# Optimization experiments

Hardware: AMD Instinct MI355X
Metric: run time of the kernel (lower is better)

## Reference

```python
import jax, jax.numpy as jnp
import numpy as np

B, N, D, E, H, K = 2, 2048, 1024, 8, 2048, 2


def setup_inputs() -> dict:
    key = jax.random.key(0)
    ks = jax.random.split(key, 5)
    s = 0.02  # init scale
    return {
        "x": jax.random.normal(ks[0], (B, N, D), dtype=jnp.float32),
        "w_gate": jax.random.normal(ks[1], (D, E), dtype=jnp.float32) * s,
        "b_gate": jnp.zeros((E,), dtype=jnp.float32),
        "w1": jax.random.normal(ks[2], (E, D, H), dtype=jnp.float32) * s,
        "b1": jnp.zeros((E, H), dtype=jnp.float32),
        "w2": jax.random.normal(ks[3], (E, H, D), dtype=jnp.float32) * s,
        "b2": jnp.zeros((E, D), dtype=jnp.float32),
    }


def reference(x, w_gate, b_gate, w1, b1, w2, b2):
    b, n, d = x.shape
    T = b * n
    xf = x.reshape(T, d)                                   # (T, D)
    # --- top-k routing ---
    logits = xf @ w_gate + b_gate                          # (T, E)
    topk_logits, topk_idx = jax.lax.top_k(logits, K)       # (T, K)
    topk_gates = jax.nn.softmax(topk_logits, axis=-1)      # softmax over selected experts
    entropy = -(topk_gates * jnp.log(jnp.clip(topk_gates, 1e-8, None))).sum(-1).mean()
    # scatter top-k gates into full (T, E) gate matrix (zeros for unselected)
    gates = jnp.zeros_like(logits).at[jnp.arange(T)[:, None], topk_idx].add(topk_gates)
    # --- expert MLPs (dense over experts; gates zero out unselected) ---
    h = jax.nn.relu(jnp.einsum('td,edh->eth', xf, w1) + b1[:, None, :])  # (E, T, H)
    y = jnp.einsum('eth,ehd->etd', h, w2) + b2[:, None, :]               # (E, T, D)
    out = jnp.einsum('etd,te->td', y, gates).reshape(b, n, d)
    return out, entropy
```

## Files before the change

### kernel.cpp

```cpp
#include <hip/hip_runtime.h>

#define T_TOK 4096
#define D_DIM 1024
#define E_EXP 8
#define H_DIM 2048
#define CAP   9216
#define TILES_M 72

typedef __attribute__((ext_vector_type(8))) short bf16x8;
typedef __attribute__((ext_vector_type(4))) float f32x4;

__device__ inline unsigned short f2bf(float f) {
    unsigned int u = __float_as_uint(f);
    unsigned int r = (u + 0x7fffu + ((u >> 16) & 1u)) >> 16;
    return (unsigned short)r;
}

#define GLD_LDS16(g, l)                                                        \
    __builtin_amdgcn_global_load_lds(                                          \
        (const __attribute__((address_space(1))) void*)(g),                    \
        (__attribute__((address_space(3))) void*)(l), 16, 0, 0)

__global__ __launch_bounds__(256) void tcvt_kernel(const float* __restrict__ src,
                                                   unsigned short* __restrict__ dst,
                                                   int R, int C) {
    __shared__ float tile[64][65];
    size_t eo = (size_t)blockIdx.z * R * C;
    src += eo; dst += eo;
    int tx = threadIdx.x & 15, ty = threadIdx.x >> 4;
    int c0 = blockIdx.x * 64, r0 = blockIdx.y * 64;
    #pragma unroll
    for (int i = 0; i < 4; i++) {
        int row = ty + i * 16;
        float4 v = *(const float4*)&src[(size_t)(r0 + row) * C + c0 + tx * 4];
        tile[row][tx * 4 + 0] = v.x;
        tile[row][tx * 4 + 1] = v.y;
        tile[row][tx * 4 + 2] = v.z;
        tile[row][tx * 4 + 3] = v.w;
    }
    __syncthreads();
    #pragma unroll
    for (int i = 0; i < 4; i++) {
        int cc = ty + i * 16;
        int rr = tx * 4;
        ushort4 o;
        o.x = f2bf(tile[rr + 0][cc]);
        o.y = f2bf(tile[rr + 1][cc]);
        o.z = f2bf(tile[rr + 2][cc]);
        o.w = f2bf(tile[rr + 3][cc]);
        *(ushort4*)&dst[(size_t)(c0 + cc) * R + r0 + rr] = o;
    }
}

__global__ __launch_bounds__(256) void gating_kernel(
    const float* __restrict__ xf, const float* __restrict__ wg,
    const float* __restrict__ bg, unsigned short* __restrict__ xb,
    int* __restrict__ tk_e, float* __restrict__ tk_g,
    float* __restrict__ ent_part)
{
    __shared__ float ents[4];
    int wave = threadIdx.x >> 6, lane = threadIdx.x & 63;
    int t = blockIdx.x * 4 + wave;
    const float* xr = xf + (size_t)t * D_DIM;
    unsigned short* xbr = xb + (size_t)t * D_DIM;
    float acc[8] = {0.f,0.f,0.f,0.f,0.f,0.f,0.f,0.f};
    for (int i = 0; i < 16; i++) {
        int d = lane + i * 64;
        float xv = xr[d];
        xbr[d] = f2bf(xv);
        const float4* wr = (const float4*)(wg + (size_t)d * 8);
        float4 w0 = wr[0], w1 = wr[1];
        acc[0] += xv * w0.x; acc[1] += xv * w0.y; acc[2] += xv * w0.z; acc[3] += xv * w0.w;
        acc[4] += xv * w1.x; acc[5] += xv * w1.y; acc[6] += xv * w1.z; acc[7] += xv * w1.w;
    }
    #pragma unroll
    for (int s = 1; s < 64; s <<= 1) {
        #pragma unroll
        for (int e = 0; e < 8; e++) acc[e] += __shfl_xor(acc[e], s, 64);
    }
    if (lane == 0) {
        float l[8];
        #pragma unroll
        for (int e = 0; e < 8; e++) l[e] = acc[e] + bg[e];
        int i0 = 0;
        #pragma unroll
        for (int e = 1; e < 8; e++) if (l[e] > l[i0]) i0 = e;
        int i1 = (i0 == 0) ? 1 : 0;
        #pragma unroll
        for (int e = 0; e < 8; e++) if (e != i0 && l[e] > l[i1]) i1 = e;
        float z  = expf(l[i1] - l[i0]);
        float p0 = 1.0f / (1.0f + z);
        float p1 = z / (1.0f + z);
        float ent = -(p0 * logf(fmaxf(p0, 1e-8f)) + p1 * logf(fmaxf(p1, 1e-8f)));
        ents[wave] = ent;
        tk_e[t * 2 + 0] = i0; tk_g[t * 2 + 0] = p0;
        tk_e[t * 2 + 1] = i1; tk_g[t * 2 + 1] = p1;
    }
    __syncthreads();
    if (threadIdx.x == 0)
        ent_part[blockIdx.x] = ents[0] + ents[1] + ents[2] + ents[3];
}

__global__ __launch_bounds__(1024) void route_kernel(
    const int* __restrict__ tk_e, const float* __restrict__ tk_g,
    int* __restrict__ off, int* __restrict__ slot_token,
    float* __restrict__ slot_gate, int* __restrict__ slot_of,
    const float* __restrict__ ent_part, float* __restrict__ ent_out)
{
    __shared__ int wt[16][8];
    __shared__ int wx[16][8];
    __shared__ int base[9];
    __shared__ int tot[8];
    __shared__ float es[16];

    int tid = threadIdx.x, wid = tid >> 6, lane = tid & 63;
    int i0 = tid * 8;
    int ev[8];
    *(int4*)&ev[0] = *(const int4*)&tk_e[i0];
    *(int4*)&ev[4] = *(const int4*)&tk_e[i0 + 4];

    float s = ent_part[tid];
    #pragma unroll
    for (int d = 1; d < 64; d <<= 1) s += __shfl_xor(s, d, 64);
    if (lane == 0) es[wid] = s;

    unsigned own[4] = {0u, 0u, 0u, 0u};
    #pragma unroll
    for (int j = 0; j < 8; j++) {
        int e = ev[j];
        int reg = ((e < 4) ? 0 : 2) + (e & 1);
        own[reg] += 1u << (((e >> 1) & 1) * 16);
    }
    unsigned inc[4] = {own[0], own[1], own[2], own[3]};
    #pragma unroll
    for (int d = 1; d < 64; d <<= 1) {
        #pragma unroll
        for (int k = 0; k < 4; k++) {
            unsigned t = __shfl_up(inc[k], d, 64);
            if (lane >= d) inc[k] += t;
        }
    }
    if (lane == 63) {
        #pragma unroll
        for (int e = 0; e < 8; e++) {
            int reg = ((e < 4) ? 0 : 2) + (e & 1);
            wt[wid][e] = (inc[reg] >> (((e >> 1) & 1) * 16)) & 0xFFFF;
        }
    }
    __syncthreads();
    if (tid == 0) {
        int o = 0;
        for (int e = 0; e < 8; e++) {
            int run = 0;
            for (int w = 0; w < 16; w++) { wx[w][e] = run; run += wt[w][e]; }
            tot[e] = run;
            base[e] = o;
            off[e] = o;
            o += (run + 127) & ~127;
        }
        base[8] = o;
        off[8] = o;
        float se = 0.f;
        for (int w = 0; w < 16; w++) se += es[w];
        *ent_out = se * (1.0f / T_TOK);
    }
    __syncthreads();

    #pragma unroll
    for (int e = 0; e < 8; e++) {
        int p0 = base[e] + tot[e], p1 = base[e + 1];
        for (int i = p0 + tid; i < p1; i += 1024) slot_token[i] = -1;
    }

    unsigned run[4] = {0u, 0u, 0u, 0u};
    #pragma unroll
    for (int j = 0; j < 8; j++) {
        int e = ev[j];
        int reg = ((e < 4) ? 0 : 2) + (e & 1);
        int sh = ((e >> 1) & 1) * 16;
        int lx = (int)(((inc[reg] - own[reg]) >> sh) & 0xFFFF);
        int lr = (int)((run[reg] >> sh) & 0xFFFF);
        int slot = base[e] + wx[wid][e] + lx + lr;
        run[reg] += 1u << sh;
        int i = i0 + j;
        slot_token[slot] = i >> 1;
        slot_gate[slot] = tk_g[i];
        slot_of[i] = slot;
    }
}

__global__ __launch_bounds__(256) void gemm1_kernel(
    const unsigned short* __restrict__ xb, const unsigned short* __restrict__ w1t,
    const float* __restrict__ b1g, const int* __restrict__ off,
    const int* __restrict__ slot_token, unsigned short* __restrict__ Hb)
{
    __shared__ __align__(16) unsigned short As[128 * 32];
    __shared__ __align__(16) unsigned short Bs[128 * 32];

    int s0 = blockIdx.x * 128;
    if (s0 >= off[E_EXP]) return;
    int e = 0;
    while (s0 >= off[e + 1]) e++;
    int n0 = blockIdx.y * 128;

    int tid = threadIdx.x;
    int wave = tid >> 6, lane = tid & 63;
    int lrow = lane & 15, quad = lane >> 4;
    int srow = lane >> 2;
    int scol = ((lane & 3) ^ ((srow >> 1) & 3)) * 8;

    int r0 = 16 * wave + srow, r1 = r0 + 64;
    int t0 = slot_token[s0 + r0]; if (t0 < 0) t0 = 0;
    int t1 = slot_token[s0 + r1]; if (t1 < 0) t1 = 0;
    const unsigned short* wb = w1t + (size_t)e * H_DIM * D_DIM;
    const unsigned short* a0 = xb + (size_t)t0 * D_DIM + scol;
    const unsigned short* a1 = xb + (size_t)t1 * D_DIM + scol;
    const unsigned short* bp0 = wb + (size_t)(n0 + r0) * D_DIM + scol;
    const unsigned short* bp1 = wb + (size_t)(n0 + r1) * D_DIM + scol;

    unsigned short* lA0 = As + (16 * wave) * 32;
    unsigned short* lA1 = As + (64 + 16 * wave) * 32;
    unsigned short* lB0 = Bs + (16 * wave) * 32;
    unsigned short* lB1 = Bs + (64 + 16 * wave) * 32;

    f32x4 acc[4][4];
    #pragma unroll
    for (int mi = 0; mi < 4; mi++)
        #pragma unroll
        for (int ni = 0; ni < 4; ni++) acc[mi][ni] = (f32x4){0.f, 0.f, 0.f, 0.f};

    int wr = (wave >> 1) * 64, wc = (wave & 1) * 64;
    int g = (quad ^ ((lrow >> 1) & 3)) * 8;

    for (int k0 = 0; k0 < D_DIM; k0 += 32) {
        __syncthreads();
        GLD_LDS16(a0 + k0, lA0);
        GLD_LDS16(a1 + k0, lA1);
        GLD_LDS16(bp0 + k0, lB0);
        GLD_LDS16(bp1 + k0, lB1);
        __syncthreads();
        bf16x8 af[4], bfr[4];
        #pragma unroll
        for (int i = 0; i < 4; i++) {
            af[i]  = *(const bf16x8*)&As[(wr + i * 16 + lrow) * 32 + g];
            bfr[i] = *(const bf16x8*)&Bs[(wc + i * 16 + lrow) * 32 + g];
        }
        #pragma unroll
        for (int mi = 0; mi < 4; mi++)
            #pragma unroll
            for (int ni = 0; ni < 4; ni++)
                acc[mi][ni] = __builtin_amdgcn_mfma_f32_16x16x32_bf16(
                    af[mi], bfr[ni], acc[mi][ni], 0, 0, 0);
    }

    float bv[4];
    #pragma unroll
    for (int ni = 0; ni < 4; ni++) bv[ni] = b1g[e * H_DIM + n0 + wc + ni * 16 + lrow];
    unsigned short* w = As + wave * 1024;
    __syncthreads();
    #pragma unroll
    for (int mi = 0; mi < 4; mi++) {
        #pragma unroll
        for (int ni = 0; ni < 4; ni++)
            #pragma unroll
            for (int r = 0; r < 4; r++)
                w[(quad * 4 + r) * 64 + ni * 16 + lrow] =
                    f2bf(fmaxf(acc[mi][ni][r] + bv[ni], 0.0f));
        int rd = lane >> 3, cc = (lane & 7) * 8;
        bf16x8 v0 = *(const bf16x8*)&w[rd * 64 + cc];
        bf16x8 v1 = *(const bf16x8*)&w[(8 + rd) * 64 + cc];
        size_t rowg = (size_t)(s0 + wr + mi * 16 + rd) * H_DIM + n0 + wc + cc;
        *(bf16x8*)&Hb[rowg] = v0;
        *(bf16x8*)&Hb[rowg + 8 * H_DIM] = v1;
    }
}

__global__ __launch_bounds__(256) void gemm2_kernel(
    const unsigned short* __restrict__ Hb, const unsigned short* __restrict__ w2t,
    const float* __restrict__ b2g, const int* __restrict__ off,
    unsigned short* __restrict__ Yb)
{
    __shared__ __align__(16) unsigned short As[128 * 32];
    __shared__ __align__(16) unsigned short Bs[128 * 32];

    int s0 = blockIdx.x * 128;
    if (s0 >= off[E_EXP]) return;
    int e = 0;
    while (s0 >= off[e + 1]) e++;
    int n0 = blockIdx.y * 128;

    int tid = threadIdx.x;
    int wave = tid >> 6, lane = tid & 63;
    int lrow = lane & 15, quad = lane >> 4;
    int srow = lane >> 2;
    int scol = ((lane & 3) ^ ((srow >> 1) & 3)) * 8;

    int r0 = 16 * wave + srow, r1 = r0 + 64;
    const unsigned short* wb = w2t + (size_t)e * D_DIM * H_DIM;
    const unsigned short* a0 = Hb + (size_t)(s0 + r0) * H_DIM + scol;
    const unsigned short* a1 = Hb + (size_t)(s0 + r1) * H_DIM + scol;
    const unsigned short* bp0 = wb + (size_t)(n0 + r0) * H_DIM + scol;
    const unsigned short* bp1 = wb + (size_t)(n0 + r1) * H_DIM + scol;

    unsigned short* lA0 = As + (16 * wave) * 32;
    unsigned short* lA1 = As + (64 + 16 * wave) * 32;
    unsigned short* lB0 = Bs + (16 * wave) * 32;
    unsigned short* lB1 = Bs + (64 + 16 * wave) * 32;

    f32x4 acc[4][4];
    #pragma unroll
    for (int mi = 0; mi < 4; mi++)
        #pragma unroll
        for (int ni = 0; ni < 4; ni++) acc[mi][ni] = (f32x4){0.f, 0.f, 0.f, 0.f};

    int wr = (wave >> 1) * 64, wc = (wave & 1) * 64;
    int g = (quad ^ ((lrow >> 1) & 3)) * 8;

    for (int k0 = 0; k0 < H_DIM; k0 += 32) {
        __syncthreads();
        GLD_LDS16(a0 + k0, lA0);
        GLD_LDS16(a1 + k0, lA1);
        GLD_LDS16(bp0 + k0, lB0);
        GLD_LDS16(bp1 + k0, lB1);
        __syncthreads();
        bf16x8 af[4], bfr[4];
        #pragma unroll
        for (int i = 0; i < 4; i++) {
            af[i]  = *(const bf16x8*)&As[(wr + i * 16 + lrow) * 32 + g];
            bfr[i] = *(const bf16x8*)&Bs[(wc + i * 16 + lrow) * 32 + g];
        }
        #pragma unroll
        for (int mi = 0; mi < 4; mi++)
            #pragma unroll
            for (int ni = 0; ni < 4; ni++)
                acc[mi][ni] = __builtin_amdgcn_mfma_f32_16x16x32_bf16(
                    af[mi], bfr[ni], acc[mi][ni], 0, 0, 0);
    }

    float bv[4];
    #pragma unroll
    for (int ni = 0; ni < 4; ni++) bv[ni] = b2g[e * D_DIM + n0 + wc + ni * 16 + lrow];
    unsigned short* w = As + wave * 1024;
    __syncthreads();
    #pragma unroll
    for (int mi = 0; mi < 4; mi++) {
        #pragma unroll
        for (int ni = 0; ni < 4; ni++)
            #pragma unroll
            for (int r = 0; r < 4; r++)
                w[(quad * 4 + r) * 64 + ni * 16 + lrow] = f2bf(acc[mi][ni][r] + bv[ni]);
        int rd = lane >> 3, cc = (lane & 7) * 8;
        bf16x8 v0 = *(const bf16x8*)&w[rd * 64 + cc];
        bf16x8 v1 = *(const bf16x8*)&w[(8 + rd) * 64 + cc];
        size_t rowg = (size_t)(s0 + wr + mi * 16 + rd) * D_DIM + n0 + wc + cc;
        *(bf16x8*)&Yb[rowg] = v0;
        *(bf16x8*)&Yb[rowg + 8 * D_DIM] = v1;
    }
}

__global__ __launch_bounds__(256) void combine_kernel(
    const unsigned short* __restrict__ Yb, const int* __restrict__ slot_of,
    const float* __restrict__ tk_g, float* __restrict__ out)
{
    int t = blockIdx.x * 2 + (threadIdx.x >> 7);
    int j = threadIdx.x & 127;
    int sA = slot_of[t * 2], sB = slot_of[t * 2 + 1];
    float gA = tk_g[t * 2], gB = tk_g[t * 2 + 1];
    uint4 va = *(const uint4*)(Yb + (size_t)sA * D_DIM + j * 8);
    uint4 vb = *(const uint4*)(Yb + (size_t)sB * D_DIM + j * 8);
    const unsigned int* pa = (const unsigned int*)&va;
    const unsigned int* pb = (const unsigned int*)&vb;
    float o[8];
    #pragma unroll
    for (int i = 0; i < 4; i++) {
        float a_lo = __uint_as_float(pa[i] << 16);
        float a_hi = __uint_as_float(pa[i] & 0xffff0000u);
        float b_lo = __uint_as_float(pb[i] << 16);
        float b_hi = __uint_as_float(pb[i] & 0xffff0000u);
        o[i * 2 + 0] = gA * a_lo + gB * b_lo;
        o[i * 2 + 1] = gA * a_hi + gB * b_hi;
    }
    float* op = out + (size_t)t * D_DIM + j * 8;
    ((float4*)op)[0] = make_float4(o[0], o[1], o[2], o[3]);
    ((float4*)op)[1] = make_float4(o[4], o[5], o[6], o[7]);
}

extern "C" void kernel_launch(void* const* d_in, const int* in_sizes, int n_in,
                              void* d_out, int out_size, void* d_ws, size_t ws_size,
                              hipStream_t stream)
{
    const float* xf = (const float*)d_in[0];
    const float* wg = (const float*)d_in[1];
    const float* bg = (const float*)d_in[2];
    const float* w1 = (const float*)d_in[3];
    const float* b1 = (const float*)d_in[4];
    const float* w2 = (const float*)d_in[5];
    const float* b2 = (const float*)d_in[6];
    float* out = (float*)d_out;

    char* p = (char*)d_ws;
    int* off    = (int*)p;
    int* tk_e   = off + 16;
    float* tk_g = (float*)(tk_e + T_TOK * 2);
    int* slot_token = (int*)(tk_g + T_TOK * 2);
    float* slot_gate = (float*)(slot_token + CAP);
    int* slot_of = (int*)(slot_gate + CAP);
    float* ent_part = (float*)(slot_of + T_TOK * 2);
    size_t ofs = ((size_t)((char*)(ent_part + T_TOK / 4) - p) + 255) & ~(size_t)255;
    unsigned short* xb  = (unsigned short*)(p + ofs); ofs += (size_t)T_TOK * D_DIM * 2;
    unsigned short* w1t = (unsigned short*)(p + ofs); ofs += (size_t)E_EXP * D_DIM * H_DIM * 2;
    unsigned short* w2t = (unsigned short*)(p + ofs); ofs += (size_t)E_EXP * H_DIM * D_DIM * 2;
    unsigned short* Hb  = (unsigned short*)(p + ofs); ofs += (size_t)CAP * H_DIM * 2;
    unsigned short* Yb  = w1t;

    gating_kernel<<<T_TOK / 4, 256, 0, stream>>>(xf, wg, bg, xb, tk_e, tk_g, ent_part);
    route_kernel<<<1, 1024, 0, stream>>>(tk_e, tk_g, off, slot_token, slot_gate, slot_of,
                                         ent_part, out + (size_t)T_TOK * D_DIM);
    tcvt_kernel<<<dim3(H_DIM / 64, D_DIM / 64, E_EXP), 256, 0, stream>>>(w1, w1t, D_DIM, H_DIM);
    tcvt_kernel<<<dim3(D_DIM / 64, H_DIM / 64, E_EXP), 256, 0, stream>>>(w2, w2t, H_DIM, D_DIM);
    gemm1_kernel<<<dim3(TILES_M, H_DIM / 128), 256, 0, stream>>>(xb, w1t, b1, off,
                                                                 slot_token, Hb);
    gemm2_kernel<<<dim3(TILES_M, D_DIM / 128), 256, 0, stream>>>(Hb, w2t, b2, off, Yb);
    combine_kernel<<<T_TOK / 2, 256, 0, stream>>>(Yb, slot_of, tk_g, out);
}
```

Before: 329.5 us.

## Fuse prep kernels and double-buffer LDS in expert GEMMs

Merges the gating and both weight transpose-convert kernels into one launch, dropping two launches and letting gating overlap the transposes. The gating loop now reads contiguous float4 chunks per lane and writes bf16 in 16-byte stores. Both GEMMs get double-buffered LDS with prefetch of the next K tile and one barrier per iteration, and use a 1D grid with the N tile varying fastest so blocks sharing a token tile run together. Doubling LDS may lower occupancy, and the single-barrier scheme depends on the async LDS loads having completed by the next barrier.

```diff
diff --git a/kernel.cpp b/kernel.cpp
--- a/kernel.cpp
+++ b/kernel.cpp
@@ -21,14 +21,88 @@
         (const __attribute__((address_space(1))) void*)(g),                    \
         (__attribute__((address_space(3))) void*)(l), 16, 0, 0)
 
-__global__ __launch_bounds__(256) void tcvt_kernel(const float* __restrict__ src,
-                                                   unsigned short* __restrict__ dst,
-                                                   int R, int C) {
+__global__ __launch_bounds__(256) void prep_kernel(
+    const float* __restrict__ xf, const float* __restrict__ wg,
+    const float* __restrict__ bg, unsigned short* __restrict__ xb,
+    int* __restrict__ tk_e, float* __restrict__ tk_g,
+    float* __restrict__ ent_part,
+    const float* __restrict__ w1, unsigned short* __restrict__ w1t,
+    const float* __restrict__ w2, unsigned short* __restrict__ w2t)
+{
     __shared__ float tile[64][65];
-    size_t eo = (size_t)blockIdx.z * R * C;
+    int id = blockIdx.x;
+
+    if (id < 1024) {
+        int wave = threadIdx.x >> 6, lane = threadIdx.x & 63;
+        int t = id * 4 + wave;
+        const float* xr = xf + (size_t)t * D_DIM;
+        unsigned short* xbr = xb + (size_t)t * D_DIM;
+        float acc[8] = {0.f,0.f,0.f,0.f,0.f,0.f,0.f,0.f};
+        int d0 = lane * 16;
+        unsigned short ob[16];
+        #pragma unroll
+        for (int j = 0; j < 16; j += 4) {
+            float4 xv = *(const float4*)&xr[d0 + j];
+            float xs[4] = {xv.x, xv.y, xv.z, xv.w};
+            #pragma unroll
+            for (int jj = 0; jj < 4; jj++) {
+                int d = d0 + j + jj;
+                float x = xs[jj];
+                ob[j + jj] = f2bf(x);
+                const float4* wr = (const float4*)(wg + (size_t)d * 8);
+                float4 w0 = wr[0], w1v = wr[1];
+                acc[0] += x * w0.x;  acc[1] += x * w0.y;
+                acc[2] += x * w0.z;  acc[3] += x * w0.w;
+                acc[4] += x * w1v.x; acc[5] += x * w1v.y;
+                acc[6] += x * w1v.z; acc[7] += x * w1v.w;
+            }
+        }
+        *(uint4*)&xbr[d0]     = *(uint4*)&ob[0];
+        *(uint4*)&xbr[d0 + 8] = *(uint4*)&ob[8];
+        #pragma unroll
+        for (int s = 1; s < 64; s <<= 1) {
+            #pragma unroll
+            for (int e = 0; e < 8; e++) acc[e] += __shfl_xor(acc[e], s, 64);
+        }
+        float* ents = (float*)tile;
+        if (lane == 0) {
+            float l[8];
+            #pragma unroll
+            for (int e = 0; e < 8; e++) l[e] = acc[e] + bg[e];
+            int i0 = 0;
+            #pragma unroll
+            for (int e = 1; e < 8; e++) if (l[e] > l[i0]) i0 = e;
+            int i1 = (i0 == 0) ? 1 : 0;
+            #pragma unroll
+            for (int e = 0; e < 8; e++) if (e != i0 && l[e] > l[i1]) i1 = e;
+            float z  = expf(l[i1] - l[i0]);
+            float p0 = 1.0f / (1.0f + z);
+            float p1 = z / (1.0f + z);
+            float ent = -(p0 * logf(fmaxf(p0, 1e-8f)) + p1 * logf(fmaxf(p1, 1e-8f)));
+            ents[wave] = ent;
+            tk_e[t * 2 + 0] = i0; tk_g[t * 2 + 0] = p0;
+            tk_e[t * 2 + 1] = i1; tk_g[t * 2 + 1] = p1;
+        }
+        __syncthreads();
+        if (threadIdx.x == 0)
+            ent_part[id] = ents[0] + ents[1] + ents[2] + ents[3];
+        return;
+    }
+
+    const float* src; unsigned short* dst; int R, C, bx, by, bz;
+    if (id < 1024 + 4096) {
+        int i2 = id - 1024;
+        bx = i2 & 31; by = (i2 >> 5) & 15; bz = i2 >> 9;
+        src = w1; dst = w1t; R = D_DIM; C = H_DIM;
+    } else {
+        int i3 = id - (1024 + 4096);
+        bx = i3 & 15; by = (i3 >> 4) & 31; bz = i3 >> 9;
+        src = w2; dst = w2t; R = H_DIM; C = D_DIM;
+    }
+    size_t eo = (size_t)bz * R * C;
     src += eo; dst += eo;
     int tx = threadIdx.x & 15, ty = threadIdx.x >> 4;
-    int c0 = blockIdx.x * 64, r0 = blockIdx.y * 64;
+    int c0 = bx * 64, r0 = by * 64;
     #pragma unroll
     for (int i = 0; i < 4; i++) {
         int row = ty + i * 16;
@@ -50,55 +124,6 @@
         o.w = f2bf(tile[rr + 3][cc]);
         *(ushort4*)&dst[(size_t)(c0 + cc) * R + r0 + rr] = o;
     }
-}
-
-__global__ __launch_bounds__(256) void gating_kernel(
-    const float* __restrict__ xf, const float* __restrict__ wg,
-    const float* __restrict__ bg, unsigned short* __restrict__ xb,
-    int* __restrict__ tk_e, float* __restrict__ tk_g,
-    float* __restrict__ ent_part)
-{
-    __shared__ float ents[4];
-    int wave = threadIdx.x >> 6, lane = threadIdx.x & 63;
-    int t = blockIdx.x * 4 + wave;
-    const float* xr = xf + (size_t)t * D_DIM;
-    unsigned short* xbr = xb + (size_t)t * D_DIM;
-    float acc[8] = {0.f,0.f,0.f,0.f,0.f,0.f,0.f,0.f};
-    for (int i = 0; i < 16; i++) {
-        int d = lane + i * 64;
-        float xv = xr[d];
-        xbr[d] = f2bf(xv);
-        const float4* wr = (const float4*)(wg + (size_t)d * 8);
-        float4 w0 = wr[0], w1 = wr[1];
-        acc[0] += xv * w0.x; acc[1] += xv * w0.y; acc[2] += xv * w0.z; acc[3] += xv * w0.w;
-        acc[4] += xv * w1.x; acc[5] += xv * w1.y; acc[6] += xv * w1.z; acc[7] += xv * w1.w;
-    }
-    #pragma unroll
-    for (int s = 1; s < 64; s <<= 1) {
-        #pragma unroll
-        for (int e = 0; e < 8; e++) acc[e] += __shfl_xor(acc[e], s, 64);
-    }
-    if (lane == 0) {
-        float l[8];
-        #pragma unroll
-        for (int e = 0; e < 8; e++) l[e] = acc[e] + bg[e];
-        int i0 = 0;
-        #pragma unroll
-        for (int e = 1; e < 8; e++) if (l[e] > l[i0]) i0 = e;
-        int i1 = (i0 == 0) ? 1 : 0;
-        #pragma unroll
-        for (int e = 0; e < 8; e++) if (e != i0 && l[e] > l[i1]) i1 = e;
-        float z  = expf(l[i1] - l[i0]);
-        float p0 = 1.0f / (1.0f + z);
-        float p1 = z / (1.0f + z);
-        float ent = -(p0 * logf(fmaxf(p0, 1e-8f)) + p1 * logf(fmaxf(p1, 1e-8f)));
-        ents[wave] = ent;
-        tk_e[t * 2 + 0] = i0; tk_g[t * 2 + 0] = p0;
-        tk_e[t * 2 + 1] = i1; tk_g[t * 2 + 1] = p1;
-    }
-    __syncthreads();
-    if (threadIdx.x == 0)
-        ent_part[blockIdx.x] = ents[0] + ents[1] + ents[2] + ents[3];
 }
 
 __global__ __launch_bounds__(1024) void route_kernel(
@@ -194,14 +219,15 @@
     const float* __restrict__ b1g, const int* __restrict__ off,
     const int* __restrict__ slot_token, unsigned short* __restrict__ Hb)
 {
-    __shared__ __align__(16) unsigned short As[128 * 32];
-    __shared__ __align__(16) unsigned short Bs[128 * 32];
-
-    int s0 = blockIdx.x * 128;
+    __shared__ __align__(16) unsigned short As[2 * 128 * 32];
+    __shared__ __align__(16) unsigned short Bs[2 * 128 * 32];
+
+    int id = blockIdx.x;
+    int s0 = (id >> 4) * 128;
+    int n0 = (id & 15) * 128;
     if (s0 >= off[E_EXP]) return;
     int e = 0;
     while (s0 >= off[e + 1]) e++;
-    int n0 = blockIdx.y * 128;
 
     int tid = threadIdx.x;
     int wave = tid >> 6, lane = tid & 63;
@@ -218,10 +244,8 @@
     const unsigned short* bp0 = wb + (size_t)(n0 + r0) * D_DIM + scol;
     const unsigned short* bp1 = wb + (size_t)(n0 + r1) * D_DIM + scol;
 
-    unsigned short* lA0 = As + (16 * wave) * 32;
-    unsigned short* lA1 = As + (64 + 16 * wave) * 32;
-    unsigned short* lB0 = Bs + (16 * wave) * 32;
-    unsigned short* lB1 = Bs + (64 + 16 * wave) * 32;
+    int w0 = (16 * wave) * 32;
+    int w1o = (64 + 16 * wave) * 32;
 
     f32x4 acc[4][4];
     #pragma unroll
@@ -232,18 +256,29 @@
     int wr = (wave >> 1) * 64, wc = (wave & 1) * 64;
     int g = (quad ^ ((lrow >> 1) & 3)) * 8;
 
+    GLD_LDS16(a0, As + w0);
+    GLD_LDS16(a1, As + w1o);
+    GLD_LDS16(bp0, Bs + w0);
+    GLD_LDS16(bp1, Bs + w1o);
+
     for (int k0 = 0; k0 < D_DIM; k0 += 32) {
+        int cur = (k0 >> 5) & 1;
+        unsigned short* Ac = As + cur * 4096;
+        unsigned short* Bc = Bs + cur * 4096;
         __syncthreads();
-        GLD_LDS16(a0 + k0, lA0);
-        GLD_LDS16(a1 + k0, lA1);
-        GLD_LDS16(bp0 + k0, lB0);
-        GLD_LDS16(bp1 + k0, lB1);
-        __syncthreads();
+        if (k0 + 32 < D_DIM) {
+            unsigned short* An = As + (cur ^ 1) * 4096;
+            unsigned short* Bn = Bs + (cur ^ 1) * 4096;
+            GLD_LDS16(a0 + k0 + 32, An + w0);
+            GLD_LDS16(a1 + k0 + 32, An + w1o);
+            GLD_LDS16(bp0 + k0 + 32, Bn + w0);
+            GLD_LDS16(bp1 + k0 + 32, Bn + w1o);
+        }
         bf16x8 af[4], bfr[4];
         #pragma unroll
         for (int i = 0; i < 4; i++) {
-            af[i]  = *(const bf16x8*)&As[(wr + i * 16 + lrow) * 32 + g];
-            bfr[i] = *(const bf16x8*)&Bs[(wc + i * 16 + lrow) * 32 + g];
+            af[i]  = *(const bf16x8*)&Ac[(wr + i * 16 + lrow) * 32 + g];
+            bfr[i] = *(const bf16x8*)&Bc[(wc + i * 16 + lrow) * 32 + g];
         }
         #pragma unroll
         for (int mi = 0; mi < 4; mi++)
@@ -280,14 +315,15 @@
     const float* __restrict__ b2g, const int* __restrict__ off,
     unsigned short* __restrict__ Yb)
 {
-    __shared__ __align__(16) unsigned short As[128 * 32];
-    __shared__ __align__(16) unsigned short Bs[128 * 32];
-
-    int s0 = blockIdx.x * 128;
+    __shared__ __align__(16) unsigned short As[2 * 128 * 32];
+    __shared__ __align__(16) unsigned short Bs[2 * 128 * 32];
+
+    int id = blockIdx.x;
+    int s0 = (id >> 3) * 128;
+    int n0 = (id & 7) * 128;
     if (s0 >= off[E_EXP]) return;
     int e = 0;
     while (s0 >= off[e + 1]) e++;
-    int n0 = blockIdx.y * 128;
 
     int tid = threadIdx.x;
     int wave = tid >> 6, lane = tid & 63;
@@ -302,10 +338,8 @@
     const unsigned short* bp0 = wb + (size_t)(n0 + r0) * H_DIM + scol;
     const unsigned short* bp1 = wb + (size_t)(n0 + r1) * H_DIM + scol;
 
-    unsigned short* lA0 = As + (16 * wave) * 32;
-    unsigned short* lA1 = As + (64 + 16 * wave) * 32;
-    unsigned short* lB0 = Bs + (16 * wave) * 32;
-    unsigned short* lB1 = Bs + (64 + 16 * wave) * 32;
+    int w0 = (16 * wave) * 32;
+    int w1o = (64 + 16 * wave) * 32;
 
     f32x4 acc[4][4];
     #pragma unroll
@@ -316,18 +350,29 @@
     int wr = (wave >> 1) * 64, wc = (wave & 1) * 64;
     int g = (quad ^ ((lrow >> 1) & 3)) * 8;
 
+    GLD_LDS16(a0, As + w0);
+    GLD_LDS16(a1, As + w1o);
+    GLD_LDS16(bp0, Bs + w0);
+    GLD_LDS16(bp1, Bs + w1o);
+
     for (int k0 = 0; k0 < H_DIM; k0 += 32) {
+        int cur = (k0 >> 5) & 1;
+        unsigned short* Ac = As + cur * 4096;
+        unsigned short* Bc = Bs + cur * 4096;
         __syncthreads();
-        GLD_LDS16(a0 + k0, lA0);
-        GLD_LDS16(a1 + k0, lA1);
-        GLD_LDS16(bp0 + k0, lB0);
-        GLD_LDS16(bp1 + k0, lB1);
-        __syncthreads();
+        if (k0 + 32 < H_DIM) {
+            unsigned short* An = As + (cur ^ 1) * 4096;
+            unsigned short* Bn = Bs + (cur ^ 1) * 4096;
+            GLD_LDS16(a0 + k0 + 32, An + w0);
+            GLD_LDS16(a1 + k0 + 32, An + w1o);
+            GLD_LDS16(bp0 + k0 + 32, Bn + w0);
+            GLD_LDS16(bp1 + k0 + 32, Bn + w1o);
+        }
         bf16x8 af[4], bfr[4];
         #pragma unroll
         for (int i = 0; i < 4; i++) {
-            af[i]  = *(const bf16x8*)&As[(wr + i * 16 + lrow) * 32 + g];
-            bfr[i] = *(const bf16x8*)&Bs[(wc + i * 16 + lrow) * 32 + g];
+            af[i]  = *(const bf16x8*)&Ac[(wr + i * 16 + lrow) * 32 + g];
+            bfr[i] = *(const bf16x8*)&Bc[(wc + i * 16 + lrow) * 32 + g];
         }
         #pragma unroll
         for (int mi = 0; mi < 4; mi++)
@@ -413,13 +458,11 @@
     unsigned short* Hb  = (unsigned short*)(p + ofs); ofs += (size_t)CAP * H_DIM * 2;
     unsigned short* Yb  = w1t;
 
-    gating_kernel<<<T_TOK / 4, 256, 0, stream>>>(xf, wg, bg, xb, tk_e, tk_g, ent_part);
+    prep_kernel<<<1024 + 4096 + 4096, 256, 0, stream>>>(
+        xf, wg, bg, xb, tk_e, tk_g, ent_part, w1, w1t, w2, w2t);
     route_kernel<<<1, 1024, 0, stream>>>(tk_e, tk_g, off, slot_token, slot_gate, slot_of,
                                          ent_part, out + (size_t)T_TOK * D_DIM);
-    tcvt_kernel<<<dim3(H_DIM / 64, D_DIM / 64, E_EXP), 256, 0, stream>>>(w1, w1t, D_DIM, H_DIM);
-    tcvt_kernel<<<dim3(D_DIM / 64, H_DIM / 64, E_EXP), 256, 0, stream>>>(w2, w2t, H_DIM, D_DIM);
-    gemm1_kernel<<<dim3(TILES_M, H_DIM / 128), 256, 0, stream>>>(xb, w1t, b1, off,
-                                                                 slot_token, Hb);
-    gemm2_kernel<<<dim3(TILES_M, D_DIM / 128), 256, 0, stream>>>(Hb, w2t, b2, off, Yb);
+    gemm1_kernel<<<TILES_M * 16, 256, 0, stream>>>(xb, w1t, b1, off, slot_token, Hb);
+    gemm2_kernel<<<TILES_M * 8, 256, 0, stream>>>(Hb, w2t, b2, off, Yb);
     combine_kernel<<<T_TOK / 2, 256, 0, stream>>>(Yb, slot_of, tk_g, out);
 }
```

After: 334.6 us. About the same (+1.6%).
